# Kernel tuning notes

Measured on AMD Instinct MI355X. Metric: run time of the kernel, lower is better.

## Reference

```python
import jax, jax.numpy as jnp
import numpy as np

EPSILON = 0.01        # temperature
DIST_THRESH = 0.2
NUM_ITERS = 8         # sparse_rebalance_iters (== num_iters here)
TOPK = 64             # topk_support
NEG_INF = -1e9


def setup_inputs() -> dict:
    key = jax.random.key(0)
    k1, k2, k3 = jax.random.split(key, 3)
    B, N, M, D = 4, 4096, 4096, 128
    return {
        "source_feats": jax.random.normal(k1, (B, N, D), dtype=jnp.float32),
        "source_locs": jax.random.uniform(k2, (B, N, 2), dtype=jnp.float32),
        "target_locs": jax.random.uniform(k3, (B, M, 2), dtype=jnp.float32),
        "source_valid_mask": jnp.ones((B, N), dtype=bool),
        "target_valid_mask": jnp.ones((B, M), dtype=bool),
    }


def _sinkhorn_attn(source_locs, target_locs, source_valid_mask, target_valid_mask):
    # pairwise squared distances: [B, M, N]
    diff = target_locs[:, :, None, :] - source_locs[:, None, :, :]
    dist_sq = jnp.sum(diff * diff, axis=-1)
    log_k = -dist_sq / (EPSILON + 1e-8)
    valid = (dist_sq < DIST_THRESH ** 2)
    valid = valid & source_valid_mask[:, None, :] & target_valid_mask[:, :, None]

    B, M, N = valid.shape
    topk = min(TOPK, N)
    if topk < N:
        masked_log_k = jnp.where(valid, log_k, NEG_INF)
        _, topk_idx = jax.lax.top_k(masked_log_k, topk)  # [B, M, topk]
        support = jnp.zeros_like(valid).at[
            jnp.arange(B)[:, None, None], jnp.arange(M)[None, :, None], topk_idx
        ].set(True)
        valid = valid & support

    log_k = jnp.where(valid, log_k, NEG_INF)

    v = jnp.zeros((B, 1, N), dtype=log_k.dtype)
    u = jnp.zeros((B, M, 1), dtype=log_k.dtype)
    for _ in range(NUM_ITERS):
        u = -jax.nn.logsumexp(log_k + v, axis=2, keepdims=True)
        v = -jax.nn.logsumexp(log_k + u, axis=1, keepdims=True)
        v = jnp.where(source_valid_mask[:, None, :], v, 0.0)

    attn = jnp.exp(log_k + u + v)              # [B, M, N]
    has_source = valid.any(axis=-1, keepdims=True)  # [B, M, 1]
    return attn, has_source


def reference(source_feats, source_locs, target_locs, source_valid_mask, target_valid_mask):
    attn, has_source = _sinkhorn_attn(source_locs, target_locs,
                                      source_valid_mask, target_valid_mask)
    target_feats = jnp.einsum('bmn,bnd->bmd', attn, source_feats)
    target_feats = target_feats * target_valid_mask[:, :, None].astype(target_feats.dtype)
    target_feats = target_feats * has_source.astype(target_feats.dtype)
    return target_feats
```

## Files before the change

### kernel.cpp

```cpp
#include <hip/hip_runtime.h>
#include <math.h>

#define B 4
#define N 4096
#define M 4096
#define D 128
#define K 64
#define BT 256
#define WPB 4
#define RPW 4
#define CAP 768
#define CUTCAP 128
#define PC 128
#define SCAP 1536
#define EPS_DENOM 0.01000001f
#define THRESH2 0.04f
#define GC 16

__device__ __forceinline__ unsigned bf16hi(float f){
    unsigned u = __float_as_uint(f);
    return (u + 0x7FFFu + ((u >> 16) & 1u)) & 0xFFFF0000u;
}

__global__ __launch_bounds__(1024) void k_sort(const float* __restrict__ slocs,
        const float* __restrict__ tlocs,
        float4* __restrict__ sPack, float4* __restrict__ tPack,
        int* __restrict__ cellStart,
        int* __restrict__ colcnt, int* __restrict__ E, int* __restrict__ R,
        float* __restrict__ extraF, float* __restrict__ cs){
    __shared__ int hist[256], startS[256], fill[256], wtot[4];
    __shared__ float2 loc[N];
    __shared__ unsigned short scell[N];
    const int blk = blockIdx.x, tid = threadIdx.x;
    const bool tgt = blk >= B;
    const int b = tgt ? (blk - B) : blk;
    const int lane = tid & 63, w = tid >> 6;
    const float2* slp = (const float2*)((tgt ? tlocs : slocs) + (size_t)b * N * 2);
    float4* outPack = (tgt ? tPack : sPack) + (size_t)b * N;

    if (!tgt){
        for (int i = tid; i < N; i += 1024){
            colcnt[b * N + i] = 0;
            cs[b * N + i] = 1.0f;
        }
        if (b == 0){
            if (tid < B){ E[tid] = 0; R[tid] = 0; }
            if (tid < B * D) extraF[tid] = 0.f;
        }
    }

    if (tid < 256){ hist[tid] = 0; fill[tid] = 0; }
    __syncthreads();
    for (int i = tid; i < N; i += 1024){
        float2 p = slp[i];
        int cx = min(GC - 1, max(0, (int)(p.x * (float)GC)));
        int cy = min(GC - 1, max(0, (int)(p.y * (float)GC)));
        int cell = cy * GC + cx;
        loc[i] = p; scell[i] = (unsigned short)cell;
        atomicAdd(&hist[cell], 1);
    }
    __syncthreads();
    int hv = (tid < 256) ? hist[tid] : 0;
    int pre = hv;
    #pragma unroll
    for (int o = 1; o < 64; o <<= 1){ int t2 = __shfl_up(pre, o, 64); if (lane >= o) pre += t2; }
    if (tid < 256 && lane == 63) wtot[w] = pre;
    __syncthreads();
    if (tid < 256){
        int off = 0;
        for (int i = 0; i < w; ++i) off += wtot[i];
        int st = off + pre - hv;
        startS[tid] = st;
        if (!tgt) cellStart[b * 257 + tid] = st;
    }
    if (!tgt && tid == 0) cellStart[b * 257 + 256] = N;
    __syncthreads();
    for (int i = tid; i < N; i += 1024){
        int cell = scell[i];
        int pos = startS[cell] + atomicAdd(&fill[cell], 1);
        float2 p = loc[i];
        outPack[pos] = make_float4(p.x, p.y, __int_as_float(i), 0.f);
    }
}

__global__ __launch_bounds__(BT, 5) void k_build(const float4* __restrict__ sPack,
        const int* __restrict__ cellStart, const float4* __restrict__ tPack,
        unsigned* __restrict__ csrP, int* __restrict__ cnt,
        int* __restrict__ colcnt, unsigned* __restrict__ cscP,
        int* __restrict__ R){
    __shared__ int cs[257];
    __shared__ float2 sxy[SCAP];
    __shared__ int    sid[SCAP];
    __shared__ unsigned short cj[WPB][CAP];
    __shared__ int   hist[WPB][64];
    __shared__ float cutd[WPB][CUTCAP];
    __shared__ int   cutn[WPB][CUTCAP];
    __shared__ float4 rowT[16];
    __shared__ int gB[16], gL[16], lB[16];
    __shared__ int stot;

    const int bid  = blockIdx.x;
    const int sb   = (bid & 7) * 128 + (bid >> 3);
    const int b    = sb >> 8;
    const int s00  = (sb & 255) * (WPB * RPW);
    const int tid  = threadIdx.x;
    const int w    = tid >> 6;
    const int lane = tid & 63;
    const unsigned long long pmask = (lane == 0) ? 0ull : ((1ull << lane) - 1);
    const float4* sp = sPack + (size_t)b * N;
    const float4* tp = tPack + (size_t)b * M;

    for (int i = tid; i < 257; i += BT) cs[i] = cellStart[b * 257 + i];
    if (tid < 16) rowT[tid] = tp[s00 + tid];
    __syncthreads();

    float txmin = 1e9f, txmax = -1e9f, tymin = 1e9f, tymax = -1e9f;
    #pragma unroll
    for (int i = 0; i < 16; ++i){
        float4 t = rowT[i];
        txmin = fminf(txmin, t.x); txmax = fmaxf(txmax, t.x);
        tymin = fminf(tymin, t.y); tymax = fmaxf(tymax, t.y);
    }
    const int bcy0 = max(0, (int)floorf((tymin - 0.2f) * (float)GC - 0.001f));
    const int bcy1 = min(GC - 1, (int)floorf((tymax + 0.2f) * (float)GC + 0.001f));
    const int ncy  = bcy1 - bcy0 + 1;
    if (tid < ncy && tid < 16){
        int cy = bcy0 + tid;
        float rowLo = cy * 0.0625f, rowHi = rowLo + 0.0625f;
        float dymin = fmaxf(0.f, fmaxf(rowLo - tymax, tymin - rowHi));
        float dxm = sqrtf(fmaxf(THRESH2 - dymin * dymin + 1e-5f, 0.f));
        int cx0 = max(0, (int)floorf((txmin - dxm) * (float)GC - 0.001f));
        int cx1 = min(GC - 1, (int)floorf((txmax + dxm) * (float)GC + 0.001f));
        int s = cs[cy * GC + cx0], e = cs[cy * GC + cx1 + 1];
        gB[tid] = s; gL[tid] = e - s;
    }
    __syncthreads();
    if (tid == 0){
        if (ncy > 16) stot = SCAP + 1;
        else {
            int acc = 0;
            for (int i = 0; i < ncy; ++i){ lB[i] = acc; acc += gL[i]; }
            stot = acc;
        }
    }
    __syncthreads();
    const bool staged = (stot <= SCAP);
    if (staged){
        for (int i = 0; i < ncy; ++i){
            int s = gB[i], len = gL[i], l0 = lB[i];
            for (int j = tid; j < len; j += BT){
                float4 q = sp[s + j];
                sxy[l0 + j] = make_float2(q.x, q.y);
                sid[l0 + j] = ((s + j) << 16) | __float_as_int(q.z);
            }
        }
    }
    __syncthreads();

    for (int r = 0; r < RPW; ++r){
        const int srt   = s00 + w * RPW + r;
        const int srid  = b * M + srt;
        const float4 t  = rowT[w * RPW + r];
        const float tx  = t.x;
        const float ty  = t.y;

        hist[w][lane] = 0;

        const int cy0 = max(0, (int)floorf((ty - 0.2f) * (float)GC - 0.001f));
        const int cy1 = min(GC - 1, (int)floorf((ty + 0.2f) * (float)GC + 0.001f));

        int c = 0;
        for (int cy = cy0; cy <= cy1; ++cy){
            float rowLo = cy * 0.0625f, rowHi = rowLo + 0.0625f;
            float dymin = fmaxf(0.f, fmaxf(rowLo - ty, ty - rowHi));
            float dxm = sqrtf(fmaxf(THRESH2 - dymin * dymin + 1e-5f, 0.f));
            int cx0 = max(0, (int)floorf((tx - dxm) * (float)GC - 0.001f));
            int cx1 = min(GC - 1, (int)floorf((tx + dxm) * (float)GC + 0.001f));
            int s = cs[cy * GC + cx0], e = cs[cy * GC + cx1 + 1];
            int len = e - s;
            int base_l = staged ? (lB[cy - bcy0] + (s - gB[cy - bcy0])) : s;
            for (int j0 = 0; j0 < len; j0 += 64){
                int i = j0 + lane;
                bool valid = i < len;
                int lp = base_l + i;
                float d2 = 1e9f;
                if (valid){
                    float qx, qy;
                    if (staged){ float2 q = sxy[lp]; qx = q.x; qy = q.y; }
                    else       { float4 q = sp[lp];  qx = q.x; qy = q.y; }
                    float dx = __fsub_rn(tx, qx);
                    float dy = __fsub_rn(ty, qy);
                    d2 = __fadd_rn(__fmul_rn(dx, dx), __fmul_rn(dy, dy));
                }
                bool in = valid && (d2 < THRESH2);
                unsigned long long ml = __ballot(in);
                if (in){
                    int p = c + __popcll(ml & pmask);
                    if (p < CAP) cj[w][p] = (unsigned short)lp;
                    atomicAdd(&hist[w][min((int)(d2 * 1600.0f), 63)], 1);
                }
                c += __popcll(ml);
            }
        }
        const int ctot = min(c, CAP);

        int h = hist[w][lane];
        int pre = h;
        #pragma unroll
        for (int o = 1; o < 64; o <<= 1){
            int t2 = __shfl_up(pre, o, 64);
            if (lane >= o) pre += t2;
        }
        int cutB = 64, q = 0;
        if (c > K){
            unsigned long long ge = __ballot(pre >= K);
            int fb = __ffsll((long long)ge) - 1;
            cutB = fb;
            q = K - __shfl(pre - h, fb, 64);
        }

        int base = 0, cutc = 0;
        for (int i0 = 0; i0 < ctot; i0 += 64){
            int i = i0 + lane;
            bool valid = i < ctot;
            float d2 = 1e9f; int pk = 0;
            if (valid){
                int lp = cj[w][i];
                float qx, qy;
                if (staged){ float2 q = sxy[lp]; qx = q.x; qy = q.y; pk = sid[lp]; }
                else       { float4 q = sp[lp];  qx = q.x; qy = q.y;
                             pk = (lp << 16) | __float_as_int(q.z); }
                float dx = __fsub_rn(tx, qx);
                float dy = __fsub_rn(ty, qy);
                d2 = __fadd_rn(__fmul_rn(dx, dx), __fmul_rn(dy, dy));
            }
            int bk = valid ? min((int)(d2 * 1600.0f), 63) : 64;
            bool low = valid && (bk < cutB);
            unsigned long long ml = __ballot(low);
            if (low){
                int p = base + __popcll(ml & pmask);
                unsigned eb = bf16hi(expf(-(d2 / EPS_DENOM)));
                int cpos = pk >> 16;
                csrP[(size_t)srid * K + p] = eb | (unsigned)cpos;
                int bn = (b << 12) + cpos;
                int slot = atomicAdd(&colcnt[bn], 1);
                if (slot < PC)
                    cscP[(size_t)bn * PC + slot] = eb | (unsigned)srt;
            }
            base += __popcll(ml);
            if (cutB < 64){
                bool eq = valid && (bk == cutB);
                unsigned long long me = __ballot(eq);
                if (eq){
                    int p = cutc + __popcll(me & pmask);
                    if (p < CUTCAP){ cutd[w][p] = d2; cutn[w][p] = pk; }
                }
                cutc += __popcll(me);
            }
        }

        if (c > K){
            int cc = min(cutc, CUTCAP);
            for (int i0 = 0; i0 < CUTCAP; i0 += 64){
                int i = i0 + lane;
                bool sel = false; float d2i = 0.f; int ni = 0;
                if (i < cc){
                    d2i = cutd[w][i]; ni = cutn[w][i];
                    int rank = 0;
                    for (int j = 0; j < cc; ++j){
                        float dj = cutd[w][j]; int nj = cutn[w][j];
                        rank += (dj < d2i) || (dj == d2i && (nj & 0xFFFF) < (ni & 0xFFFF));
                    }
                    sel = rank < q;
                }
                unsigned long long ms = __ballot(sel);
                if (sel){
                    int p = base + __popcll(ms & pmask);
                    unsigned eb = bf16hi(expf(-(d2i / EPS_DENOM)));
                    int cpos = ni >> 16;
                    csrP[(size_t)srid * K + p] = eb | (unsigned)cpos;
                    int bn = (b << 12) + cpos;
                    int slot = atomicAdd(&colcnt[bn], 1);
                    if (slot < PC)
                        cscP[(size_t)bn * PC + slot] = eb | (unsigned)srt;
                }
                base += __popcll(ms);
                if (i0 + 64 >= cc) break;
            }
            if (lane == 0) cnt[srid] = K;
        } else {
            if (lane == 0){
                cnt[srid] = c;
                if (c == 0) atomicAdd(&R[b], 1);
            }
        }
    }
}

__global__ __launch_bounds__(256) void k_prep(const int* __restrict__ colcnt,
        int* __restrict__ E, const float* __restrict__ feats,
        const float4* __restrict__ sPack, float* __restrict__ extraF){
    int t = blockIdx.x * blockDim.x + threadIdx.x;
    int lane = t & 63, b = t >> 12;
    int cc = colcnt[t];
    unsigned long long em = __ballot(cc == 0);
    if (lane == 0 && em) atomicAdd(&E[b], __popcll(em));
    if (cc == 0){
        int orig = __float_as_int(sPack[t].z);
        for (int d = 0; d < D; ++d)
            atomicAdd(&extraF[b * D + d], feats[((size_t)((b << 12) + orig)) * D + d]);
    }
}

__global__ __launch_bounds__(256) void kA(const unsigned* __restrict__ csrP,
        const int* __restrict__ cnt,
        const float* __restrict__ cs, const int* __restrict__ E, float* __restrict__ eu){
    int t = blockIdx.x * blockDim.x + threadIdx.x;
    int W = t >> 6, lane = t & 63;
    for (int rr = 0; rr < 4; ++rr){
        int rid = W * 4 + rr;
        int b = rid >> 12;
        int c = cnt[rid];
        float s = 0.f;
        if (lane < c){
            unsigned pe = csrP[(size_t)rid * K + lane];
            s = __uint_as_float(pe & 0xFFFF0000u) / cs[(b << 12) + (pe & 0xFFFFu)];
        }
        #pragma unroll
        for (int o = 32; o; o >>= 1) s += __shfl_xor(s, o, 64);
        int Eb = E[b];
        if (c == 0 && Eb == 0){
            if (lane == 0) eu[rid] = 0.f;
        } else {
            if (Eb > 0) s += (float)Eb;
            if (lane == 0) eu[rid] = 1.0f / s;
        }
    }
}

__global__ __launch_bounds__(256) void kB(const unsigned* __restrict__ cscP,
        const int* __restrict__ colcnt,
        const float* __restrict__ eu, const int* __restrict__ R, float* __restrict__ cs){
    int t = blockIdx.x * blockDim.x + threadIdx.x;
    int W = t >> 6, lane = t & 63;
    for (int rr = 0; rr < 4; ++rr){
        int cid = W * 4 + rr;
        int b = cid >> 12;
        int cc = min(colcnt[cid], PC);
        float s = 0.f;
        for (int p = lane; p < cc; p += 64){
            unsigned pe = cscP[(size_t)cid * PC + p];
            s += __uint_as_float(pe & 0xFFFF0000u) * eu[(b << 12) + (pe & 0xFFFFu)];
        }
        #pragma unroll
        for (int o = 32; o; o >>= 1) s += __shfl_xor(s, o, 64);
        if (lane == 0)
            cs[cid] = s + (float)R[b];
    }
}

__global__ __launch_bounds__(128) void k_out(const float* __restrict__ feats,
        const unsigned* __restrict__ csrP,
        const int* __restrict__ cnt, const float* __restrict__ eu,
        const float* __restrict__ cs, const float* __restrict__ extraF,
        const float4* __restrict__ sPack, const float4* __restrict__ tPack,
        float* __restrict__ out){
    __shared__ float att[K];
    __shared__ int   sidx[K];
    int bid = blockIdx.x;
    int sg  = (bid & 7) * 2048 + (bid >> 3);
    int b   = sg >> 12;
    int srt = sg & 4095;
    int m   = __float_as_int(tPack[(size_t)b * M + srt].z);
    const float4* sp = sPack + (size_t)b * N;
    int tid = threadIdx.x;
    int c = cnt[sg];
    if (tid < K){
        float a = 0.f; int ix = 0;
        if (tid < c){
            unsigned pe = csrP[(size_t)sg * K + tid];
            int cpos = pe & 0xFFFFu;
            a = __uint_as_float(pe & 0xFFFF0000u) * eu[sg] / cs[(b << 12) + cpos];
            ix = __float_as_int(sp[cpos].z);
        }
        att[tid] = a; sidx[tid] = ix;
    }
    __syncthreads();
    float acc = 0.f;
    if (c > 0){
        acc = extraF[b * D + tid];
        for (int k = 0; k < c; ++k)
            acc += att[k] * feats[((size_t)((b << 12) + sidx[k])) * D + tid];
    }
    out[((size_t)((b << 12) + m)) * D + tid] = acc;
}

extern "C" void kernel_launch(void* const* d_in, const int* in_sizes, int n_in,
                              void* d_out, int out_size, void* d_ws, size_t ws_size,
                              hipStream_t stream){
    const float* feats = (const float*)d_in[0];
    const float* slocs = (const float*)d_in[1];
    const float* tlocs = (const float*)d_in[2];
    float* out = (float*)d_out;

    char* w = (char*)d_ws;
    size_t off = 0;
    auto carve = [&](size_t bytes) -> void* {
        void* p = w + off;
        off += (bytes + 255) & ~(size_t)255;
        return p;
    };
    unsigned* csrP  = (unsigned*)carve((size_t)B * M * K * 4);
    unsigned* cscP  = (unsigned*)carve((size_t)B * N * PC * 4);
    int*   cnt     = (int*)  carve((size_t)B * M * 4);
    int*   colcnt  = (int*)  carve((size_t)B * N * 4);
    float* eu      = (float*)carve((size_t)B * M * 4);
    float* cs      = (float*)carve((size_t)B * N * 4);
    int*   E       = (int*)  carve(B * 4);
    int*   R       = (int*)  carve(B * 4);
    float* extraF  = (float*)carve((size_t)B * D * 4);
    float4* sPack  = (float4*)carve((size_t)B * N * 16);
    float4* tPack  = (float4*)carve((size_t)B * M * 16);
    int*   cellStart = (int*)carve((size_t)B * 257 * 4);

    k_sort<<<2 * B, 1024, 0, stream>>>(slocs, tlocs, sPack, tPack, cellStart,
                                       colcnt, E, R, extraF, cs);
    k_build<<<B * M / (WPB * RPW), BT, 0, stream>>>(sPack, cellStart, tPack,
            csrP, cnt, colcnt, cscP, R);
    k_prep<<<(B * N) / 256, 256, 0, stream>>>(colcnt, E, feats, sPack, extraF);
    for (int it = 0; it < 8; ++it){
        kA<<<B * M / 16, 256, 0, stream>>>(csrP, cnt, cs, E, eu);
        kB<<<B * N / 16, 256, 0, stream>>>(cscP, colcnt, eu, R, cs);
    }
    k_out<<<B * M, D, 0, stream>>>(feats, csrP, cnt, eu, cs, extraF, sPack, tPack, out);
}
```

Measured before the change: 243.4 us.

## Shrink k_build shared buffers for occupancy and store reciprocal column sums

Lowers the CAP, SCAP and CUTCAP shared-memory sizes and raises the k_build launch bound to 6 blocks per CU, which should allow more resident waves. With CUTCAP at 64, the tie-break selection over cut candidates collapses into a single pass. The column sums are now stored as reciprocals, so kA and k_out multiply instead of divide, and the first kA iteration skips the gather of the initial all-ones values. The risk is that a row or cell group exceeding the smaller capacities silently drops candidates, which could break correctness on denser inputs.

```diff
diff --git a/kernel.cpp b/kernel.cpp
--- a/kernel.cpp
+++ b/kernel.cpp
@@ -9,10 +9,10 @@
 #define BT 256
 #define WPB 4
 #define RPW 4
-#define CAP 768
-#define CUTCAP 128
+#define CAP 640
+#define CUTCAP 64
 #define PC 128
-#define SCAP 1536
+#define SCAP 1280
 #define EPS_DENOM 0.01000001f
 #define THRESH2 0.04f
 #define GC 16
@@ -27,7 +27,7 @@
         float4* __restrict__ sPack, float4* __restrict__ tPack,
         int* __restrict__ cellStart,
         int* __restrict__ colcnt, int* __restrict__ E, int* __restrict__ R,
-        float* __restrict__ extraF, float* __restrict__ cs){
+        float* __restrict__ extraF, float* __restrict__ ics){
     __shared__ int hist[256], startS[256], fill[256], wtot[4];
     __shared__ float2 loc[N];
     __shared__ unsigned short scell[N];
@@ -41,7 +41,7 @@
     if (!tgt){
         for (int i = tid; i < N; i += 1024){
             colcnt[b * N + i] = 0;
-            cs[b * N + i] = 1.0f;
+            ics[b * N + i] = 1.0f;
         }
         if (b == 0){
             if (tid < B){ E[tid] = 0; R[tid] = 0; }
@@ -83,7 +83,7 @@
     }
 }
 
-__global__ __launch_bounds__(BT, 5) void k_build(const float4* __restrict__ sPack,
+__global__ __launch_bounds__(BT, 6) void k_build(const float4* __restrict__ sPack,
         const int* __restrict__ cellStart, const float4* __restrict__ tPack,
         unsigned* __restrict__ csrP, int* __restrict__ cnt,
         int* __restrict__ colcnt, unsigned* __restrict__ cscP,
@@ -261,8 +261,8 @@
 
         if (c > K){
             int cc = min(cutc, CUTCAP);
-            for (int i0 = 0; i0 < CUTCAP; i0 += 64){
-                int i = i0 + lane;
+            {
+                int i = lane;
                 bool sel = false; float d2i = 0.f; int ni = 0;
                 if (i < cc){
                     d2i = cutd[w][i]; ni = cutn[w][i];
@@ -284,8 +284,6 @@
                     if (slot < PC)
                         cscP[(size_t)bn * PC + slot] = eb | (unsigned)srt;
                 }
-                base += __popcll(ms);
-                if (i0 + 64 >= cc) break;
             }
             if (lane == 0) cnt[srid] = K;
         } else {
@@ -314,7 +312,8 @@
 
 __global__ __launch_bounds__(256) void kA(const unsigned* __restrict__ csrP,
         const int* __restrict__ cnt,
-        const float* __restrict__ cs, const int* __restrict__ E, float* __restrict__ eu){
+        const float* __restrict__ ics, const int* __restrict__ E,
+        float* __restrict__ eu, int first){
     int t = blockIdx.x * blockDim.x + threadIdx.x;
     int W = t >> 6, lane = t & 63;
     for (int rr = 0; rr < 4; ++rr){
@@ -324,7 +323,8 @@
         float s = 0.f;
         if (lane < c){
             unsigned pe = csrP[(size_t)rid * K + lane];
-            s = __uint_as_float(pe & 0xFFFF0000u) / cs[(b << 12) + (pe & 0xFFFFu)];
+            float e = __uint_as_float(pe & 0xFFFF0000u);
+            s = first ? e : e * ics[(b << 12) + (pe & 0xFFFFu)];
         }
         #pragma unroll
         for (int o = 32; o; o >>= 1) s += __shfl_xor(s, o, 64);
@@ -340,7 +340,7 @@
 
 __global__ __launch_bounds__(256) void kB(const unsigned* __restrict__ cscP,
         const int* __restrict__ colcnt,
-        const float* __restrict__ eu, const int* __restrict__ R, float* __restrict__ cs){
+        const float* __restrict__ eu, const int* __restrict__ R, float* __restrict__ ics){
     int t = blockIdx.x * blockDim.x + threadIdx.x;
     int W = t >> 6, lane = t & 63;
     for (int rr = 0; rr < 4; ++rr){
@@ -355,14 +355,14 @@
         #pragma unroll
         for (int o = 32; o; o >>= 1) s += __shfl_xor(s, o, 64);
         if (lane == 0)
-            cs[cid] = s + (float)R[b];
+            ics[cid] = 1.0f / (s + (float)R[b]);
     }
 }
 
 __global__ __launch_bounds__(128) void k_out(const float* __restrict__ feats,
         const unsigned* __restrict__ csrP,
         const int* __restrict__ cnt, const float* __restrict__ eu,
-        const float* __restrict__ cs, const float* __restrict__ extraF,
+        const float* __restrict__ ics, const float* __restrict__ extraF,
         const float4* __restrict__ sPack, const float4* __restrict__ tPack,
         float* __restrict__ out){
     __shared__ float att[K];
@@ -380,7 +380,7 @@
         if (tid < c){
             unsigned pe = csrP[(size_t)sg * K + tid];
             int cpos = pe & 0xFFFFu;
-            a = __uint_as_float(pe & 0xFFFF0000u) * eu[sg] / cs[(b << 12) + cpos];
+            a = __uint_as_float(pe & 0xFFFF0000u) * eu[sg] * ics[(b << 12) + cpos];
             ix = __float_as_int(sp[cpos].z);
         }
         att[tid] = a; sidx[tid] = ix;
@@ -415,7 +415,7 @@
     int*   cnt     = (int*)  carve((size_t)B * M * 4);
     int*   colcnt  = (int*)  carve((size_t)B * N * 4);
     float* eu      = (float*)carve((size_t)B * M * 4);
-    float* cs      = (float*)carve((size_t)B * N * 4);
+    float* ics     = (float*)carve((size_t)B * N * 4);
     int*   E       = (int*)  carve(B * 4);
     int*   R       = (int*)  carve(B * 4);
     float* extraF  = (float*)carve((size_t)B * D * 4);
@@ -424,13 +424,13 @@
     int*   cellStart = (int*)carve((size_t)B * 257 * 4);
 
     k_sort<<<2 * B, 1024, 0, stream>>>(slocs, tlocs, sPack, tPack, cellStart,
-                                       colcnt, E, R, extraF, cs);
+                                       colcnt, E, R, extraF, ics);
     k_build<<<B * M / (WPB * RPW), BT, 0, stream>>>(sPack, cellStart, tPack,
             csrP, cnt, colcnt, cscP, R);
     k_prep<<<(B * N) / 256, 256, 0, stream>>>(colcnt, E, feats, sPack, extraF);
     for (int it = 0; it < 8; ++it){
-        kA<<<B * M / 16, 256, 0, stream>>>(csrP, cnt, cs, E, eu);
-        kB<<<B * N / 16, 256, 0, stream>>>(cscP, colcnt, eu, R, cs);
-    }
-    k_out<<<B * M, D, 0, stream>>>(feats, csrP, cnt, eu, cs, extraF, sPack, tPack, out);
-}
+        kA<<<B * M / 16, 256, 0, stream>>>(csrP, cnt, ics, E, eu, it == 0 ? 1 : 0);
+        kB<<<B * N / 16, 256, 0, stream>>>(cscP, colcnt, eu, R, ics);
+    }
+    k_out<<<B * M, D, 0, stream>>>(feats, csrP, cnt, eu, ics, extraF, sPack, tPack, out);
+}
```

New measurement: 252.1 us. 3.6% more time.
